# Optimization experiments

Measured on AMD Instinct MI355X. Metric: run time of the kernel, lower is better.

The kernel has to match this reference:

```python
import jax, jax.numpy as jnp
import numpy as np

N_NODES = 100000
N_EDGES = 1600000
IN_F, HID_F, OUT_F = 64, 64, 32


def setup_inputs() -> dict:
    key = jax.random.key(0)
    k = jax.random.split(key, 6)
    features = jax.random.normal(k[0], (N_NODES, IN_F), dtype=jnp.float32)
    src = jax.random.randint(k[1], (N_EDGES,), 0, N_NODES, dtype=jnp.int32)
    dst = jax.random.randint(k[2], (N_EDGES,), 0, N_NODES, dtype=jnp.int32)
    # Linear params (Kaiming-uniform-ish scale)
    W1 = jax.random.normal(k[3], (IN_F, HID_F), dtype=jnp.float32) / np.sqrt(IN_F)
    b1 = jnp.zeros((HID_F,), dtype=jnp.float32)
    W2 = jax.random.normal(k[4], (HID_F, OUT_F), dtype=jnp.float32) / np.sqrt(HID_F)
    b2 = jnp.zeros((OUT_F,), dtype=jnp.float32)
    return {"features": features, "src": src, "dst": dst,
            "W1": W1, "b1": b1, "W2": W2, "b2": b2}


def _graph_conv(src, dst, n_nodes, h, W, b):
    # copy_u + sum: scatter-add source features into destination nodes (SpMM)
    agg = jax.ops.segment_sum(h[src], dst, num_segments=n_nodes)
    return agg @ W + b


def reference(features, src, dst, W1, b1, W2, b2):
    n = features.shape[0]
    h = jax.nn.relu(_graph_conv(src, dst, n, features, W1, b1))
    h = _graph_conv(src, dst, n, h, W2, b2)
    return h
```

## Files before the change

kernel.cpp:

```cpp
#include <hip/hip_runtime.h>

#define N_NODES 100000
#define N_EDGES 1600000
#define NB 782
#define CAP 3072
#define EPB 8192
#define NP1 196
#define CVB 200
#define YP 72
#define AP 72
#define WINTS 3456

typedef __attribute__((ext_vector_type(8))) short bhalf8;
typedef __attribute__((ext_vector_type(4))) float f32x4;
typedef __attribute__((ext_vector_type(2))) float f32x2;

__device__ __forceinline__ unsigned short bf16r(float f) {
    unsigned u = __float_as_uint(f);
    unsigned r = (u >> 16) & 1;
    return (unsigned short)((u + 0x7fffu + r) >> 16);
}
__device__ __forceinline__ unsigned pk2(float a, float b) {
    return (unsigned)bf16r(a) | ((unsigned)bf16r(b) << 16);
}
__device__ __forceinline__ float bl(unsigned u) { return __uint_as_float(u << 16); }
__device__ __forceinline__ float bh(unsigned u) { return __uint_as_float(u & 0xffff0000u); }
__device__ __forceinline__ f32x2 ex2(unsigned u) {
    f32x2 r; r.x = __uint_as_float(u << 16); r.y = __uint_as_float(u & 0xffff0000u);
    return r;
}

__global__ __launch_bounds__(512) void prep(const float4* __restrict__ X4,
                                            uint2* __restrict__ Xb,
                                            const int* __restrict__ src,
                                            const int* __restrict__ dst,
                                            int* __restrict__ gcur,
                                            unsigned* __restrict__ ebuf,
                                            const float* __restrict__ W1,
                                            const float* __restrict__ W2,
                                            int* __restrict__ wbuf) {
    __shared__ int h[NB];
    __shared__ int lo[NB];
    __shared__ int cur[NB];
    __shared__ int wsum[8];
    __shared__ unsigned stage[EPB];
    __shared__ unsigned short bid[EPB];
    int t = threadIdx.x, lane = t & 63, wid = t >> 6;
    if (blockIdx.x >= NP1) {
        if (blockIdx.x == NP1) {
            unsigned short* wp = (unsigned short*)wbuf;
            for (int i = t; i < 64 * 64; i += 512) {
                int k = i >> 6, hc = i & 63;
                wp[hc * YP + k] = bf16r(W1[k * 64 + hc]);
            }
            for (int i = t; i < 64 * 32; i += 512) {
                int k = i >> 5, oc = i & 31;
                wp[2 * 2304 + oc * YP + k] = bf16r(W2[k * 32 + oc]);
            }
        }
        for (int i = (blockIdx.x - NP1) * 512 + t; i < N_NODES * 16; i += CVB * 512) {
            float4 v = X4[i];
            uint2 o; o.x = pk2(v.x, v.y); o.y = pk2(v.z, v.w);
            Xb[i] = o;
        }
        return;
    }
    int e0 = blockIdx.x * EPB;
    int eN = N_EDGES - e0; if (eN > EPB) eN = EPB;
    for (int b = t; b < NB; b += 512) h[b] = 0;
    __syncthreads();
    for (int i = t; i < eN; i += 512) atomicAdd(&h[dst[e0 + i] >> 7], 1);
    __syncthreads();
    int i0 = 2 * t, i1 = i0 + 1;
    int v0 = (i0 < NB) ? h[i0] : 0;
    int v1 = (i1 < NB) ? h[i1] : 0;
    int ps = v0 + v1, s = ps;
    for (int o = 1; o < 64; o <<= 1) {
        int u = __shfl_up(s, o);
        if (lane >= o) s += u;
    }
    if (lane == 63) wsum[wid] = s;
    __syncthreads();
    int wofs = 0;
    for (int w = 0; w < wid; w++) wofs += wsum[w];
    int excl = wofs + s - ps;
    if (i0 < NB) lo[i0] = excl;
    if (i1 < NB) lo[i1] = excl + v0;
    __syncthreads();
    for (int b = t; b < NB; b += 512) {
        int hb = h[b];
        int ofs = hb ? atomicAdd(&gcur[b], hb) : 0;
        h[b] = b * CAP + ofs - lo[b];
        cur[b] = lo[b];
    }
    __syncthreads();
    for (int i = t; i < eN; i += 512) {
        int sd = src[e0 + i], dd = dst[e0 + i];
        int b = dd >> 7;
        int r = atomicAdd(&cur[b], 1);
        stage[r] = ((unsigned)sd << 7) | (unsigned)(dd & 127);
        bid[r] = (unsigned short)b;
    }
    __syncthreads();
    for (int i = t; i < eN; i += 512)
        ebuf[h[bid[i]] + i] = stage[i];
}

__global__ __launch_bounds__(512, 4) void bucket1(
    unsigned* __restrict__ ebuf, const int* __restrict__ gcur,
    const uint4* __restrict__ Xb4,
    const int* __restrict__ wbuf, const float* __restrict__ b1,
    int* __restrict__ goff,
    unsigned short* __restrict__ Zb) {
    __shared__ int hh[128], nodeoff[129], scv[128];
    __shared__ unsigned short agg[128 * AP];
    __shared__ int pool[WINTS];
    int* stg = pool;
    unsigned short* sW1t = (unsigned short*)pool;
    unsigned short* sW2t = (unsigned short*)(pool + 2304);

    int b = blockIdx.x, t = threadIdx.x;
    int base = b * CAP, cnt = gcur[b];
    int lane = t & 63, wid = t >> 6;
    if (t < 128) hh[t] = 0;
    __syncthreads();
    unsigned ev[6]; int ek = 0;
    for (int i = t; i < cnt; i += 512) {
        unsigned v = ebuf[base + i];
        ev[ek++] = v;
        atomicAdd(&hh[v & 127], 1);
    }
    __syncthreads();
    if (wid == 0) {
        int v0 = hh[2 * lane], v1 = hh[2 * lane + 1];
        int ps = v0 + v1, s = ps;
        for (int o = 1; o < 64; o <<= 1) {
            int u = __shfl_up(s, o);
            if (lane >= o) s += u;
        }
        int excl = s - ps;
        nodeoff[2 * lane] = excl;
        nodeoff[2 * lane + 1] = excl + v0;
    }
    __syncthreads();
    if (t < 128) scv[t] = nodeoff[t];
    __syncthreads();
    for (int k = 0; k < ek; k++) {
        unsigned v = ev[k];
        int r = atomicAdd(&scv[v & 127], 1);
        stg[r] = (int)(v >> 7);
    }
    __syncthreads();

    for (int i = t; i < cnt; i += 512) ebuf[base + i] = (unsigned)stg[i];
    if (t < 128) goff[b * 128 + t] = nodeoff[t];

    int il = lane & 7, g = lane >> 3;
#pragma unroll
    for (int half = 0; half < 2; half++) {
        int nl = wid * 16 + half * 8 + g;
        int s0 = nodeoff[nl], d = hh[nl];
        f32x2 p0 = {0.f, 0.f}, p1 = {0.f, 0.f}, p2 = {0.f, 0.f}, p3 = {0.f, 0.f};
        int j = 0;
        for (; j + 7 < d; j += 8) {
            int s_[8];
#pragma unroll
            for (int q = 0; q < 8; q++) s_[q] = stg[s0 + j + q];
            uint4 v_[8];
#pragma unroll
            for (int q = 0; q < 8; q++) v_[q] = Xb4[s_[q] * 8 + il];
#pragma unroll
            for (int q = 0; q < 8; q++) {
                p0 += ex2(v_[q].x); p1 += ex2(v_[q].y);
                p2 += ex2(v_[q].z); p3 += ex2(v_[q].w);
            }
        }
        for (; j + 3 < d; j += 4) {
            int s_[4];
#pragma unroll
            for (int q = 0; q < 4; q++) s_[q] = stg[s0 + j + q];
            uint4 v_[4];
#pragma unroll
            for (int q = 0; q < 4; q++) v_[q] = Xb4[s_[q] * 8 + il];
#pragma unroll
            for (int q = 0; q < 4; q++) {
                p0 += ex2(v_[q].x); p1 += ex2(v_[q].y);
                p2 += ex2(v_[q].z); p3 += ex2(v_[q].w);
            }
        }
        for (; j < d; j++) {
            int sa = stg[s0 + j];
            uint4 va = Xb4[sa * 8 + il];
            p0 += ex2(va.x); p1 += ex2(va.y);
            p2 += ex2(va.z); p3 += ex2(va.w);
        }
        uint4 o;
        o.x = pk2(p0.x, p0.y); o.y = pk2(p1.x, p1.y);
        o.z = pk2(p2.x, p2.y); o.w = pk2(p3.x, p3.y);
        *(uint4*)&agg[nl * AP + il * 8] = o;
    }
    __syncthreads();

    for (int i = t; i < WINTS; i += 512) pool[i] = wbuf[i];
    __syncthreads();

    {
        int m = lane & 15, quad = lane >> 4;
        int nl = wid * 16 + m;
        int node = b * 128 + nl;
        bhalf8 Bc0 = *(const bhalf8*)&agg[nl * AP + quad * 8];
        bhalf8 Bc1 = *(const bhalf8*)&agg[nl * AP + 32 + quad * 8];
        unsigned short* ys = &agg[nl * AP];
#pragma unroll
        for (int tile = 0; tile < 4; tile++) {
            f32x4 a;
#pragma unroll
            for (int r = 0; r < 4; r++) a[r] = b1[tile * 16 + quad * 4 + r];
            bhalf8 A0 = *(const bhalf8*)&sW1t[(tile * 16 + m) * YP + quad * 8];
            bhalf8 A1 = *(const bhalf8*)&sW1t[(tile * 16 + m) * YP + 32 + quad * 8];
            a = __builtin_amdgcn_mfma_f32_16x16x32_bf16(A0, Bc0, a, 0, 0, 0);
            a = __builtin_amdgcn_mfma_f32_16x16x32_bf16(A1, Bc1, a, 0, 0, 0);
            float y0 = a[0] > 0.f ? a[0] : 0.f, y1 = a[1] > 0.f ? a[1] : 0.f;
            float y2 = a[2] > 0.f ? a[2] : 0.f, y3 = a[3] > 0.f ? a[3] : 0.f;
            uint2 o; o.x = pk2(y0, y1); o.y = pk2(y2, y3);
            *(uint2*)&ys[tile * 16 + quad * 4] = o;
        }
        __asm__ __volatile__("s_waitcnt lgkmcnt(0)" ::: "memory");
        union { bhalf8 v; uint2 u2[2]; } Y0, Y1;
        Y0.u2[0] = *(uint2*)&ys[quad * 8];
        Y0.u2[1] = *(uint2*)&ys[quad * 8 + 4];
        Y1.u2[0] = *(uint2*)&ys[32 + quad * 8];
        Y1.u2[1] = *(uint2*)&ys[32 + quad * 8 + 4];
#pragma unroll
        for (int tile = 0; tile < 2; tile++) {
            bhalf8 A0 = *(const bhalf8*)&sW2t[(tile * 16 + m) * YP + quad * 8];
            bhalf8 A1 = *(const bhalf8*)&sW2t[(tile * 16 + m) * YP + 32 + quad * 8];
            f32x4 z = {0.f, 0.f, 0.f, 0.f};
            z = __builtin_amdgcn_mfma_f32_16x16x32_bf16(A0, Y0.v, z, 0, 0, 0);
            z = __builtin_amdgcn_mfma_f32_16x16x32_bf16(A1, Y1.v, z, 0, 0, 0);
            if (node < N_NODES) {
                uint2 o; o.x = pk2(z[0], z[1]); o.y = pk2(z[2], z[3]);
                *(uint2*)&Zb[(size_t)node * 32 + tile * 16 + quad * 4] = o;
            }
        }
    }
}

__global__ __launch_bounds__(512, 4) void bucket2(
    const unsigned* __restrict__ ebuf, const int* __restrict__ gcur,
    const int* __restrict__ goff,
    const uint4* __restrict__ Zb4,
    const float* __restrict__ b2, float4* __restrict__ out4) {
    __shared__ int noff[129];
    __shared__ int stg[CAP];
    int b = blockIdx.x, t = threadIdx.x;
    int base = b * CAP, cnt = gcur[b];
    int lane = t & 63, wid = t >> 6;
    if (t < 128) noff[t] = goff[b * 128 + t];
    if (t == 128) noff[128] = cnt;
    for (int i = t; i < cnt; i += 512) stg[i] = (int)ebuf[base + i];
    __syncthreads();

    int il = lane & 3, g = lane >> 2;
    int nl = wid * 16 + g;
    int s0 = noff[nl], d = noff[nl + 1] - s0;
    f32x2 p0 = {0.f, 0.f}, p1 = {0.f, 0.f}, p2 = {0.f, 0.f}, p3 = {0.f, 0.f};
    int j = 0;
    for (; j + 7 < d; j += 8) {
        int s_[8];
#pragma unroll
        for (int q = 0; q < 8; q++) s_[q] = stg[s0 + j + q];
        uint4 v_[8];
#pragma unroll
        for (int q = 0; q < 8; q++) v_[q] = Zb4[s_[q] * 4 + il];
#pragma unroll
        for (int q = 0; q < 8; q++) {
            p0 += ex2(v_[q].x); p1 += ex2(v_[q].y);
            p2 += ex2(v_[q].z); p3 += ex2(v_[q].w);
        }
    }
    for (; j + 3 < d; j += 4) {
        int s_[4];
#pragma unroll
        for (int q = 0; q < 4; q++) s_[q] = stg[s0 + j + q];
        uint4 v_[4];
#pragma unroll
        for (int q = 0; q < 4; q++) v_[q] = Zb4[s_[q] * 4 + il];
#pragma unroll
        for (int q = 0; q < 4; q++) {
            p0 += ex2(v_[q].x); p1 += ex2(v_[q].y);
            p2 += ex2(v_[q].z); p3 += ex2(v_[q].w);
        }
    }
    for (; j < d; j++) {
        int sa = stg[s0 + j];
        uint4 va = Zb4[sa * 4 + il];
        p0 += ex2(va.x); p1 += ex2(va.y);
        p2 += ex2(va.z); p3 += ex2(va.w);
    }
    int node = b * 128 + nl;
    if (node < N_NODES) {
        float4 bbA = ((const float4*)b2)[il * 2];
        float4 bbB = ((const float4*)b2)[il * 2 + 1];
        float4 oA, oB;
        oA.x = p0.x + bbA.x; oA.y = p0.y + bbA.y; oA.z = p1.x + bbA.z; oA.w = p1.y + bbA.w;
        oB.x = p2.x + bbB.x; oB.y = p2.y + bbB.y; oB.z = p3.x + bbB.z; oB.w = p3.y + bbB.w;
        out4[node * 8 + il * 2] = oA;
        out4[node * 8 + il * 2 + 1] = oB;
    }
}

extern "C" void kernel_launch(void* const* d_in, const int* in_sizes, int n_in,
                              void* d_out, int out_size, void* d_ws, size_t ws_size,
                              hipStream_t stream) {
    const float* features = (const float*)d_in[0];
    const int*   src      = (const int*)d_in[1];
    const int*   dst      = (const int*)d_in[2];
    const float* W1       = (const float*)d_in[3];
    const float* b1       = (const float*)d_in[4];
    const float* W2       = (const float*)d_in[5];
    const float* b2       = (const float*)d_in[6];

    char* p = (char*)d_ws;
    int* gcur = (int*)p;           p += 1024 * 4;
    unsigned* ebuf = (unsigned*)p; p += (size_t)NB * CAP * 4;
    uint2* Xb = (uint2*)p;         p += (size_t)N_NODES * 64 * 2;
    unsigned short* Zb = (unsigned short*)p; p += (size_t)N_NODES * 32 * 2;
    int* wbuf = (int*)p;           p += (size_t)WINTS * 4;
    int* goff = (int*)p;           p += (size_t)NB * 128 * 4;

    hipMemsetAsync(gcur, 0, NB * sizeof(int), stream);
    prep<<<NP1 + CVB, 512, 0, stream>>>((const float4*)features, Xb, src, dst, gcur,
                                        ebuf, W1, W2, wbuf);
    bucket1<<<NB, 512, 0, stream>>>(ebuf, gcur, (const uint4*)Xb, wbuf, b1, goff, Zb);
    bucket2<<<NB, 512, 0, stream>>>(ebuf, gcur, goff, (const uint4*)Zb, b2, (float4*)d_out);
}
```

Before: 159.1 us.

## Fuse prep and both bucket kernels into one cooperative persistent kernel

Replaces three kernel launches with a single cooperative kernel of 256 blocks that runs the edge bucketing and bf16 conversion phase, the layer-1 aggregation plus MFMA transform, and the layer-2 aggregation. Grid-wide syncs separate the phases, and blocks loop over buckets persistently. The aim is to remove launch gaps and inter-kernel drain. In exchange the grid shrinks from 782 and 396 blocks to 256, which may reduce parallelism and latency hiding, and grid syncs add their own cost. The original three-kernel path is kept as a fallback if the cooperative launch fails.

New measurement: 274.3 us. 72.4% more time.

```diff
diff --git a/kernel.cpp b/kernel.cpp
--- a/kernel.cpp
+++ b/kernel.cpp
@@ -1,4 +1,7 @@
 #include <hip/hip_runtime.h>
+#include <hip/hip_cooperative_groups.h>
+
+namespace cg = cooperative_groups;
 
 #define N_NODES 100000
 #define N_EDGES 1600000
@@ -7,6 +10,7 @@
 #define EPB 8192
 #define NP1 196
 #define CVB 200
+#define GRID 256
 #define YP 72
 #define AP 72
 #define WINTS 3456
@@ -23,11 +27,290 @@
 __device__ __forceinline__ unsigned pk2(float a, float b) {
     return (unsigned)bf16r(a) | ((unsigned)bf16r(b) << 16);
 }
-__device__ __forceinline__ float bl(unsigned u) { return __uint_as_float(u << 16); }
-__device__ __forceinline__ float bh(unsigned u) { return __uint_as_float(u & 0xffff0000u); }
 __device__ __forceinline__ f32x2 ex2(unsigned u) {
     f32x2 r; r.x = __uint_as_float(u << 16); r.y = __uint_as_float(u & 0xffff0000u);
     return r;
+}
+
+__global__ __launch_bounds__(512, 4) void fused(
+    const float4* __restrict__ X4, uint2* __restrict__ Xb,
+    const int* __restrict__ src, const int* __restrict__ dst,
+    int* __restrict__ gcur, unsigned* __restrict__ ebuf,
+    const float* __restrict__ W1, const float* __restrict__ W2,
+    int* __restrict__ wbuf, const float* __restrict__ b1,
+    int* __restrict__ goff, unsigned short* __restrict__ Zb,
+    const float* __restrict__ b2, float4* __restrict__ out4) {
+    __shared__ __align__(16) char lds[58576];
+    int t = threadIdx.x, lane = t & 63, wid = t >> 6;
+    int bid = blockIdx.x;
+    const uint4* Xb4 = (const uint4*)Xb;
+    const uint4* Zb4 = (const uint4*)Zb;
+
+    if (bid < NP1) {
+        int* h   = (int*)lds;
+        int* lo  = h + NB;
+        int* cur = lo + NB;
+        int* wsum = cur + NB;
+        unsigned* stage = (unsigned*)(wsum + 8);
+        unsigned short* bidv = (unsigned short*)(stage + EPB);
+        int e0 = bid * EPB;
+        int eN = N_EDGES - e0; if (eN > EPB) eN = EPB;
+        for (int b = t; b < NB; b += 512) h[b] = 0;
+        __syncthreads();
+        for (int i = t; i < eN; i += 512) atomicAdd(&h[dst[e0 + i] >> 7], 1);
+        __syncthreads();
+        int i0 = 2 * t, i1 = i0 + 1;
+        int v0 = (i0 < NB) ? h[i0] : 0;
+        int v1 = (i1 < NB) ? h[i1] : 0;
+        int ps = v0 + v1, s = ps;
+        for (int o = 1; o < 64; o <<= 1) {
+            int u = __shfl_up(s, o);
+            if (lane >= o) s += u;
+        }
+        if (lane == 63) wsum[wid] = s;
+        __syncthreads();
+        int wofs = 0;
+        for (int w = 0; w < wid; w++) wofs += wsum[w];
+        int excl = wofs + s - ps;
+        if (i0 < NB) lo[i0] = excl;
+        if (i1 < NB) lo[i1] = excl + v0;
+        __syncthreads();
+        for (int b = t; b < NB; b += 512) {
+            int hb = h[b];
+            int ofs = hb ? atomicAdd(&gcur[b], hb) : 0;
+            h[b] = b * CAP + ofs - lo[b];
+            cur[b] = lo[b];
+        }
+        __syncthreads();
+        for (int i = t; i < eN; i += 512) {
+            int sd = src[e0 + i], dd = dst[e0 + i];
+            int b = dd >> 7;
+            int r = atomicAdd(&cur[b], 1);
+            stage[r] = ((unsigned)sd << 7) | (unsigned)(dd & 127);
+            bidv[r] = (unsigned short)b;
+        }
+        __syncthreads();
+        for (int i = t; i < eN; i += 512)
+            ebuf[h[bidv[i]] + i] = stage[i];
+    } else {
+        if (bid == NP1) {
+            unsigned short* wp = (unsigned short*)wbuf;
+            for (int i = t; i < 64 * 64; i += 512) {
+                int k = i >> 6, hc = i & 63;
+                wp[hc * YP + k] = bf16r(W1[k * 64 + hc]);
+            }
+            for (int i = t; i < 64 * 32; i += 512) {
+                int k = i >> 5, oc = i & 31;
+                wp[2 * 2304 + oc * YP + k] = bf16r(W2[k * 32 + oc]);
+            }
+        }
+        for (int i = (bid - NP1) * 512 + t; i < N_NODES * 16; i += (GRID - NP1) * 512) {
+            float4 v = X4[i];
+            uint2 o; o.x = pk2(v.x, v.y); o.y = pk2(v.z, v.w);
+            Xb[i] = o;
+        }
+    }
+    cg::this_grid().sync();
+
+    {
+        unsigned short* agg = (unsigned short*)lds;
+        int* pool = (int*)(lds + 18432);
+        int* hh = (int*)(lds + 18432 + 13824);
+        int* nodeoff = hh + 128;
+        int* scv = nodeoff + 129;
+        int* stg = pool;
+        unsigned short* sW1t = (unsigned short*)pool;
+        unsigned short* sW2t = (unsigned short*)(pool + 2304);
+
+        for (int bb = bid; bb < NB; bb += GRID) {
+            int base = bb * CAP, cnt = gcur[bb];
+            if (t < 128) hh[t] = 0;
+            __syncthreads();
+            unsigned ev[6]; int ek = 0;
+            for (int i = t; i < cnt; i += 512) {
+                unsigned v = ebuf[base + i];
+                ev[ek++] = v;
+                atomicAdd(&hh[v & 127], 1);
+            }
+            __syncthreads();
+            if (wid == 0) {
+                int v0 = hh[2 * lane], v1 = hh[2 * lane + 1];
+                int ps = v0 + v1, s = ps;
+                for (int o = 1; o < 64; o <<= 1) {
+                    int u = __shfl_up(s, o);
+                    if (lane >= o) s += u;
+                }
+                int excl = s - ps;
+                nodeoff[2 * lane] = excl;
+                nodeoff[2 * lane + 1] = excl + v0;
+            }
+            __syncthreads();
+            if (t < 128) scv[t] = nodeoff[t];
+            __syncthreads();
+            for (int k = 0; k < ek; k++) {
+                unsigned v = ev[k];
+                int r = atomicAdd(&scv[v & 127], 1);
+                stg[r] = (int)(v >> 7);
+            }
+            __syncthreads();
+
+            for (int i = t; i < cnt; i += 512) ebuf[base + i] = (unsigned)stg[i];
+            if (t < 128) goff[bb * 128 + t] = nodeoff[t];
+
+            int il = lane & 7, g = lane >> 3;
+#pragma unroll
+            for (int half = 0; half < 2; half++) {
+                int nl = wid * 16 + half * 8 + g;
+                int s0 = nodeoff[nl], d = hh[nl];
+                f32x2 p0 = {0.f, 0.f}, p1 = {0.f, 0.f}, p2 = {0.f, 0.f}, p3 = {0.f, 0.f};
+                int j = 0;
+                for (; j + 7 < d; j += 8) {
+                    int s_[8];
+#pragma unroll
+                    for (int q = 0; q < 8; q++) s_[q] = stg[s0 + j + q];
+                    uint4 v_[8];
+#pragma unroll
+                    for (int q = 0; q < 8; q++) v_[q] = Xb4[s_[q] * 8 + il];
+#pragma unroll
+                    for (int q = 0; q < 8; q++) {
+                        p0 += ex2(v_[q].x); p1 += ex2(v_[q].y);
+                        p2 += ex2(v_[q].z); p3 += ex2(v_[q].w);
+                    }
+                }
+                for (; j + 3 < d; j += 4) {
+                    int s_[4];
+#pragma unroll
+                    for (int q = 0; q < 4; q++) s_[q] = stg[s0 + j + q];
+                    uint4 v_[4];
+#pragma unroll
+                    for (int q = 0; q < 4; q++) v_[q] = Xb4[s_[q] * 8 + il];
+#pragma unroll
+                    for (int q = 0; q < 4; q++) {
+                        p0 += ex2(v_[q].x); p1 += ex2(v_[q].y);
+                        p2 += ex2(v_[q].z); p3 += ex2(v_[q].w);
+                    }
+                }
+                for (; j < d; j++) {
+                    int sa = stg[s0 + j];
+                    uint4 va = Xb4[sa * 8 + il];
+                    p0 += ex2(va.x); p1 += ex2(va.y);
+                    p2 += ex2(va.z); p3 += ex2(va.w);
+                }
+                uint4 o;
+                o.x = pk2(p0.x, p0.y); o.y = pk2(p1.x, p1.y);
+                o.z = pk2(p2.x, p2.y); o.w = pk2(p3.x, p3.y);
+                *(uint4*)&agg[nl * AP + il * 8] = o;
+            }
+            __syncthreads();
+
+            for (int i = t; i < WINTS; i += 512) pool[i] = wbuf[i];
+            __syncthreads();
+
+            {
+                int m = lane & 15, quad = lane >> 4;
+                int nl = wid * 16 + m;
+                int node = bb * 128 + nl;
+                bhalf8 Bc0 = *(const bhalf8*)&agg[nl * AP + quad * 8];
+                bhalf8 Bc1 = *(const bhalf8*)&agg[nl * AP + 32 + quad * 8];
+                unsigned short* ys = &agg[nl * AP];
+#pragma unroll
+                for (int tile = 0; tile < 4; tile++) {
+                    f32x4 a;
+#pragma unroll
+                    for (int r = 0; r < 4; r++) a[r] = b1[tile * 16 + quad * 4 + r];
+                    bhalf8 A0 = *(const bhalf8*)&sW1t[(tile * 16 + m) * YP + quad * 8];
+                    bhalf8 A1 = *(const bhalf8*)&sW1t[(tile * 16 + m) * YP + 32 + quad * 8];
+                    a = __builtin_amdgcn_mfma_f32_16x16x32_bf16(A0, Bc0, a, 0, 0, 0);
+                    a = __builtin_amdgcn_mfma_f32_16x16x32_bf16(A1, Bc1, a, 0, 0, 0);
+                    float y0 = a[0] > 0.f ? a[0] : 0.f, y1 = a[1] > 0.f ? a[1] : 0.f;
+                    float y2 = a[2] > 0.f ? a[2] : 0.f, y3 = a[3] > 0.f ? a[3] : 0.f;
+                    uint2 o; o.x = pk2(y0, y1); o.y = pk2(y2, y3);
+                    *(uint2*)&ys[tile * 16 + quad * 4] = o;
+                }
+                __asm__ __volatile__("s_waitcnt lgkmcnt(0)" ::: "memory");
+                union { bhalf8 v; uint2 u2[2]; } Y0, Y1;
+                Y0.u2[0] = *(uint2*)&ys[quad * 8];
+                Y0.u2[1] = *(uint2*)&ys[quad * 8 + 4];
+                Y1.u2[0] = *(uint2*)&ys[32 + quad * 8];
+                Y1.u2[1] = *(uint2*)&ys[32 + quad * 8 + 4];
+#pragma unroll
+                for (int tile = 0; tile < 2; tile++) {
+                    bhalf8 A0 = *(const bhalf8*)&sW2t[(tile * 16 + m) * YP + quad * 8];
+                    bhalf8 A1 = *(const bhalf8*)&sW2t[(tile * 16 + m) * YP + 32 + quad * 8];
+                    f32x4 z = {0.f, 0.f, 0.f, 0.f};
+                    z = __builtin_amdgcn_mfma_f32_16x16x32_bf16(A0, Y0.v, z, 0, 0, 0);
+                    z = __builtin_amdgcn_mfma_f32_16x16x32_bf16(A1, Y1.v, z, 0, 0, 0);
+                    if (node < N_NODES) {
+                        uint2 o; o.x = pk2(z[0], z[1]); o.y = pk2(z[2], z[3]);
+                        *(uint2*)&Zb[(size_t)node * 32 + tile * 16 + quad * 4] = o;
+                    }
+                }
+            }
+            __syncthreads();
+        }
+    }
+    cg::this_grid().sync();
+
+    {
+        int* noff = (int*)lds;
+        int* stg2 = (int*)(lds + 1024);
+        for (int bb = bid; bb < NB; bb += GRID) {
+            int base = bb * CAP, cnt = gcur[bb];
+            if (t < 128) noff[t] = goff[bb * 128 + t];
+            if (t == 128) noff[128] = cnt;
+            for (int i = t; i < cnt; i += 512) stg2[i] = (int)ebuf[base + i];
+            __syncthreads();
+
+            int il = lane & 3, g = lane >> 2;
+            int nl = wid * 16 + g;
+            int s0 = noff[nl], d = noff[nl + 1] - s0;
+            f32x2 p0 = {0.f, 0.f}, p1 = {0.f, 0.f}, p2 = {0.f, 0.f}, p3 = {0.f, 0.f};
+            int j = 0;
+            for (; j + 7 < d; j += 8) {
+                int s_[8];
+#pragma unroll
+                for (int q = 0; q < 8; q++) s_[q] = stg2[s0 + j + q];
+                uint4 v_[8];
+#pragma unroll
+                for (int q = 0; q < 8; q++) v_[q] = Zb4[s_[q] * 4 + il];
+#pragma unroll
+                for (int q = 0; q < 8; q++) {
+                    p0 += ex2(v_[q].x); p1 += ex2(v_[q].y);
+                    p2 += ex2(v_[q].z); p3 += ex2(v_[q].w);
+                }
+            }
+            for (; j + 3 < d; j += 4) {
+                int s_[4];
+#pragma unroll
+                for (int q = 0; q < 4; q++) s_[q] = stg2[s0 + j + q];
+                uint4 v_[4];
+#pragma unroll
+                for (int q = 0; q < 4; q++) v_[q] = Zb4[s_[q] * 4 + il];
+#pragma unroll
+                for (int q = 0; q < 4; q++) {
+                    p0 += ex2(v_[q].x); p1 += ex2(v_[q].y);
+                    p2 += ex2(v_[q].z); p3 += ex2(v_[q].w);
+                }
+            }
+            for (; j < d; j++) {
+                int sa = stg2[s0 + j];
+                uint4 va = Zb4[sa * 4 + il];
+                p0 += ex2(va.x); p1 += ex2(va.y);
+                p2 += ex2(va.z); p3 += ex2(va.w);
+            }
+            int node = bb * 128 + nl;
+            if (node < N_NODES) {
+                float4 bbA = ((const float4*)b2)[il * 2];
+                float4 bbB = ((const float4*)b2)[il * 2 + 1];
+                float4 oA, oB;
+                oA.x = p0.x + bbA.x; oA.y = p0.y + bbA.y; oA.z = p1.x + bbA.z; oA.w = p1.y + bbA.w;
+                oB.x = p2.x + bbB.x; oB.y = p2.y + bbB.y; oB.z = p3.x + bbB.z; oB.w = p3.y + bbB.w;
+                out4[node * 8 + il * 2] = oA;
+                out4[node * 8 + il * 2 + 1] = oB;
+            }
+            __syncthreads();
+        }
+    }
 }
 
 __global__ __launch_bounds__(512) void prep(const float4* __restrict__ X4,
@@ -330,8 +613,20 @@
     int* goff = (int*)p;           p += (size_t)NB * 128 * 4;
 
     hipMemsetAsync(gcur, 0, NB * sizeof(int), stream);
-    prep<<<NP1 + CVB, 512, 0, stream>>>((const float4*)features, Xb, src, dst, gcur,
-                                        ebuf, W1, W2, wbuf);
-    bucket1<<<NB, 512, 0, stream>>>(ebuf, gcur, (const uint4*)Xb, wbuf, b1, goff, Zb);
-    bucket2<<<NB, 512, 0, stream>>>(ebuf, gcur, goff, (const uint4*)Zb, b2, (float4*)d_out);
-}
+
+    const float4* X4 = (const float4*)features;
+    float4* out4 = (float4*)d_out;
+    void* args[] = {
+        (void*)&X4, (void*)&Xb, (void*)&src, (void*)&dst,
+        (void*)&gcur, (void*)&ebuf, (void*)&W1, (void*)&W2,
+        (void*)&wbuf, (void*)&b1, (void*)&goff, (void*)&Zb,
+        (void*)&b2, (void*)&out4,
+    };
+    hipError_t err = hipLaunchCooperativeKernel((void*)fused, dim3(GRID), dim3(512),
+                                                args, 0, stream);
+    if (err != hipSuccess) {
+        prep<<<NP1 + CVB, 512, 0, stream>>>(X4, Xb, src, dst, gcur, ebuf, W1, W2, wbuf);
+        bucket1<<<NB, 512, 0, stream>>>(ebuf, gcur, (const uint4*)Xb, wbuf, b1, goff, Zb);
+        bucket2<<<NB, 512, 0, stream>>>(ebuf, gcur, goff, (const uint4*)Zb, b2, out4);
+    }
+}
```
